# Optimization experiments

Hardware: AMD Instinct MI355X
Metric: run time of the kernel (lower is better)

Reference implementation:

```python
import jax, jax.numpy as jnp
import numpy as np

N_NODES = 100000
N_EDGES = 1600000
N_GRAPHS = 512
X_DIM = 4
H = 64
L = 3
NUM_CLASS = 3


def setup_inputs() -> dict:
    key = jax.random.key(0)
    ks = jax.random.split(key, 16)
    s = 0.1
    return {
        "x": jax.random.normal(ks[0], (N_NODES, X_DIM), jnp.float32),
        "edge_index": jax.random.randint(ks[1], (2, N_EDGES), 0, N_NODES, jnp.int64),
        "batch": jnp.sort(jax.random.randint(ks[2], (N_NODES,), 0, N_GRAPHS, jnp.int64)),
        "edge_attr": jax.random.uniform(ks[3], (N_EDGES,), jnp.float32),
        # node embedding
        "W_emb": jax.random.normal(ks[4], (X_DIM, H), jnp.float32) * s,
        "b_emb": jnp.zeros((H,), jnp.float32),
        # LEConv per-layer params (stacked over layers)
        "W1": jax.random.normal(ks[5], (L, H, H), jnp.float32) * s,
        "b1": jnp.zeros((L, H), jnp.float32),
        "W2": jax.random.normal(ks[6], (L, H, H), jnp.float32) * s,  # no bias (lin2)
        "W3": jax.random.normal(ks[7], (L, H, H), jnp.float32) * s,
        "b3": jnp.zeros((L, H), jnp.float32),
        # fc_out head
        "Wf1": jax.random.normal(ks[8], (H, 2 * H), jnp.float32) * s,
        "bf1": jnp.zeros((2 * H,), jnp.float32),
        "Wf2": jax.random.normal(ks[9], (2 * H, NUM_CLASS), jnp.float32) * s,
        "bf2": jnp.zeros((NUM_CLASS,), jnp.float32),
    }


def reference(x, edge_index, batch, edge_attr, W_emb, b_emb, W1, b1, W2, W3, b3,
              Wf1, bf1, Wf2, bf2):
    src, dst = edge_index[0], edge_index[1]
    # node embedding
    h = x @ W_emb + b_emb  # [N, H]
    # stacked LEConv layers: x_i' = sum_{j->i} e_ji * (lin1(x_j) - lin2(x_i)) + lin3(x_i)
    for l in range(L):
        a = h @ W1[l] + b1[l]          # [N, H]
        b = h @ W2[l]                  # [N, H] (lin2 has no bias)
        msg = (a[src] - b[dst]) * edge_attr[:, None]  # [E, H]
        agg = jax.ops.segment_sum(msg, dst, num_segments=N_NODES)
        h = jax.nn.relu(agg + h @ W3[l] + b3[l])
    # global mean pool per graph
    sums = jax.ops.segment_sum(h, batch, num_segments=N_GRAPHS)  # [G, H]
    cnt = jax.ops.segment_sum(jnp.ones((N_NODES,), h.dtype), batch, num_segments=N_GRAPHS)
    graph_x = sums / jnp.maximum(cnt, 1.0)[:, None]
    # fc_out head
    hid = jax.nn.relu(graph_x @ Wf1 + bf1)
    return hid @ Wf2 + bf2  # [G, NUM_CLASS]
```

## Files before the change

kernel.cpp:

```cpp
#include <hip/hip_runtime.h>

#define N_NODES 100000
#define N_EDGES 1600000
#define N_GRAPHS 512
#define X_DIM 4
#define H 64
#define LAYERS 3
#define NUM_CLASS 3
#define NBLK 256
#define EPB (N_EDGES / NBLK)
#define BKT_BITS 9
#define BKT_SZ 512
#define NBKT ((N_NODES + BKT_SZ - 1) / BKT_SZ)
#define MHIST (NBKT * NBLK)
#define NCH (MHIST / 512)
#define LROW 72
#define NCHUNKS ((N_NODES + 63) / 64)

typedef unsigned short ushort;
typedef short bf16x8 __attribute__((ext_vector_type(8)));
typedef unsigned short ush8 __attribute__((ext_vector_type(8)));
typedef float floatx4 __attribute__((ext_vector_type(4)));

__device__ __forceinline__ ushort f2bf(float v) {
    unsigned u = __float_as_uint(v);
    unsigned r = (u + 0x7fff + ((u >> 16) & 1)) >> 16;
    return (ushort)r;
}
__device__ __forceinline__ float bf2f(ushort s) {
    return __uint_as_float(((unsigned)s) << 16);
}

__global__ __launch_bounds__(256) void hist1_kernel(
    const int* __restrict__ dst, int* __restrict__ histM,
    const float* __restrict__ Wemb, const float* __restrict__ bemb,
    const float* __restrict__ W1, const float* __restrict__ b1,
    const float* __restrict__ W2, const float* __restrict__ W3,
    const float* __restrict__ b3,
    float* __restrict__ G, float* __restrict__ C) {
    __shared__ int hist[NBKT];
    int t = threadIdx.x, b = blockIdx.x;
    for (int i = t; i < NBKT; i += 256) hist[i] = 0;
    __syncthreads();
    int e0 = b * EPB;
    for (int j = t; j < EPB; j += 256) {
        int d = dst[e0 + j];
        atomicAdd(hist + (d >> BKT_BITS), 1);
    }
    __syncthreads();
    for (int i = t; i < NBKT; i += 256) histM[i * NBLK + b] = hist[i];
    if (b == 0 && t < H) {
        int f = t;
        const float* Ws[3] = {W1, W2, W3};
#pragma unroll
        for (int wsel = 0; wsel < 3; ++wsel) {
            const float* W = Ws[wsel];
#pragma unroll
            for (int c = 0; c < X_DIM; ++c) {
                float g = 0.f;
                for (int k = 0; k < H; ++k) g += Wemb[c * H + k] * W[k * H + f];
                G[wsel * 256 + c * H + f] = g;
            }
            float cb = (wsel == 0) ? b1[f] : (wsel == 2) ? b3[f] : 0.f;
            for (int k = 0; k < H; ++k) cb += bemb[k] * W[k * H + f];
            C[wsel * H + f] = cb;
        }
    }
}

__global__ __launch_bounds__(512) void gscan1_kernel(const int* __restrict__ v,
                                                     int* __restrict__ incl,
                                                     int* __restrict__ partials) {
    __shared__ int s[512];
    int tid = threadIdx.x;
    int i = blockIdx.x * 512 + tid;
    int x = (i < MHIST) ? v[i] : 0;
    s[tid] = x;
    for (int off = 1; off < 512; off <<= 1) {
        __syncthreads();
        int tv = (tid >= off) ? s[tid - off] : 0;
        __syncthreads();
        s[tid] += tv;
    }
    __syncthreads();
    if (i < MHIST) incl[i] = s[tid];
    if (tid == 511) partials[blockIdx.x] = s[tid];
}

__global__ __launch_bounds__(256) void scatter1_kernel(
    const int* __restrict__ src, const int* __restrict__ dst, const float* __restrict__ ea,
    const int* __restrict__ histM, const int* __restrict__ incl,
    const int* __restrict__ partials,
    unsigned* __restrict__ eb_se, int* __restrict__ eb_dst, int* __restrict__ bkt_ptr) {
    __shared__ int coff[128];
    __shared__ int cur[NBKT];
    int t = threadIdx.x, b = blockIdx.x;
    if (t < 128) coff[t] = (t < NCH) ? partials[t] : 0;
    __syncthreads();
    for (int off = 1; off < 128; off <<= 1) {
        int tv = (t < 128 && t >= off) ? coff[t - off] : 0;
        __syncthreads();
        if (t < 128) coff[t] += tv;
        __syncthreads();
    }
    for (int i = t; i < NBKT; i += 256) {
        int idx = i * NBLK + b;
        int ch = idx >> 9;
        int off0 = (ch == 0) ? 0 : coff[ch - 1];
        cur[i] = incl[idx] - histM[idx] + off0;
    }
    __syncthreads();
    if (b == 0) {
        for (int i = t; i < NBKT; i += 256) bkt_ptr[i] = cur[i];
        if (t == 0) bkt_ptr[NBKT] = N_EDGES;
    }
    int e0 = b * EPB;
    for (int j = t; j < EPB; j += 256) {
        int e = e0 + j;
        int d = dst[e];
        int k = d >> BKT_BITS;
        int pos = atomicAdd(cur + k, 1);
        eb_se[pos] = ((unsigned)src[e] << 15) | (unsigned)f2bf(ea[e]);
        eb_dst[pos] = d;
    }
}

__global__ __launch_bounds__(512) void bucket_kernel(
    const int* __restrict__ bkt_ptr, const unsigned* __restrict__ eb_se,
    const int* __restrict__ eb_dst,
    int* __restrict__ row_ptr, float* __restrict__ degw, unsigned* __restrict__ epack) {
    __shared__ int cnt[BKT_SZ];
    __shared__ float dws[BKT_SZ];
    __shared__ int s[BKT_SZ];
    __shared__ int cur[BKT_SZ];
    int k = blockIdx.x, t = threadIdx.x;
    int base = k << BKT_BITS;
    int nn = N_NODES - base;
    if (nn > BKT_SZ) nn = BKT_SZ;
    cnt[t] = 0;
    dws[t] = 0.0f;
    __syncthreads();
    int beg = bkt_ptr[k], end = bkt_ptr[k + 1];
    for (int j = beg + t; j < end; j += 512) {
        int d = eb_dst[j] - base;
        atomicAdd(cnt + d, 1);
        atomicAdd(dws + d, __uint_as_float((eb_se[j] & 0x7FFFu) << 16));
    }
    __syncthreads();
    s[t] = cnt[t];
    for (int off = 1; off < 512; off <<= 1) {
        __syncthreads();
        int tv = (t >= off) ? s[t - off] : 0;
        __syncthreads();
        s[t] += tv;
    }
    __syncthreads();
    int rstart = beg + s[t] - cnt[t];
    if (t < nn) {
        row_ptr[base + t] = rstart;
        degw[base + t] = dws[t];
        cur[t] = rstart;
    }
    __syncthreads();
    for (int j = beg + t; j < end; j += 512) {
        unsigned se = eb_se[j];
        int d = eb_dst[j] - base;
        int pos = atomicAdd(cur + d, 1);
        epack[pos] = se;
    }
    if (k == NBKT - 1 && t == 0) row_ptr[N_NODES] = N_EDGES;
}

__global__ __launch_bounds__(256) void layer1_kernel(
    const int* __restrict__ row_ptr, const unsigned* __restrict__ epack,
    const float* __restrict__ x, const float* __restrict__ degw,
    const float* __restrict__ G, const float* __restrict__ C,
    ushort* __restrict__ h) {
    int n = blockIdx.x * 4 + (threadIdx.x >> 6);
    if (n >= N_NODES) return;
    int lane = threadIdx.x & 63;
    float Gr[12], Cr[3];
#pragma unroll
    for (int i = 0; i < 12; ++i) Gr[i] = G[(i >> 2) * 256 + (i & 3) * 64 + lane];
#pragma unroll
    for (int i = 0; i < 3; ++i) Cr[i] = C[i * 64 + lane];
    int q2 = lane >> 1, cp = lane & 1;
    int beg = row_ptr[n], end = row_ptr[n + 1];
    float a0 = 0.f, a1 = 0.f;
    for (int j = beg; j < end; j += 32) {
        int jk = j + q2;
        unsigned w = (jk < end) ? epack[jk] : 0u;
        float2 xv = *(const float2*)&x[(size_t)(w >> 15) * X_DIM + cp * 2];
        float e = __uint_as_float((w & 0x7FFFu) << 16);
        a0 += e * xv.x;
        a1 += e * xv.y;
    }
#pragma unroll
    for (int mask = 2; mask <= 32; mask <<= 1) {
        a0 += __shfl_xor(a0, mask);
        a1 += __shfl_xor(a1, mask);
    }
    float mv0 = __shfl(a0, 0), mv1 = __shfl(a1, 0);
    float mv2 = __shfl(a0, 1), mv3 = __shfl(a1, 1);
    floatx4 xr = *(const floatx4*)&x[(size_t)n * X_DIM];
    float dw = degw[n];
    float t1 = mv0 * Gr[0] + mv1 * Gr[1] + mv2 * Gr[2] + mv3 * Gr[3];
    float t2 = xr[0] * Gr[4] + xr[1] * Gr[5] + xr[2] * Gr[6] + xr[3] * Gr[7];
    float t3 = xr[0] * Gr[8] + xr[1] * Gr[9] + xr[2] * Gr[10] + xr[3] * Gr[11];
    float v = t1 + dw * Cr[0] + t3 + Cr[2] - (t2 + Cr[1]) * dw;
    h[(size_t)n * H + lane] = f2bf(fmaxf(v, 0.0f));
}

__global__ __launch_bounds__(256) void gather_kernel(
    const int* __restrict__ row_ptr, const unsigned* __restrict__ epack,
    const ushort* __restrict__ h, ushort* __restrict__ m) {
    int n = blockIdx.x * 4 + (threadIdx.x >> 6);
    if (n >= N_NODES) return;
    int lane = threadIdx.x & 63;
    int q = lane >> 3, s = lane & 7;
    int beg = row_ptr[n], end = row_ptr[n + 1];
    float acc[8] = {0.f, 0.f, 0.f, 0.f, 0.f, 0.f, 0.f, 0.f};
    for (int j = beg; j < end; j += 32) {
        unsigned w[4];
#pragma unroll
        for (int k = 0; k < 4; ++k) {
            int jk = j + k * 8 + q;
            w[k] = (jk < end) ? epack[jk] : 0u;
        }
        ush8 av[4];
#pragma unroll
        for (int k = 0; k < 4; ++k)
            av[k] = *(const ush8*)&h[(size_t)(w[k] >> 15) * H + s * 8];
#pragma unroll
        for (int k = 0; k < 4; ++k) {
            float e = __uint_as_float((w[k] & 0x7FFFu) << 16);
#pragma unroll
            for (int i = 0; i < 8; ++i)
                acc[i] += e * bf2f((ushort)av[k][i]);
        }
    }
#pragma unroll
    for (int i = 0; i < 8; ++i) {
        acc[i] += __shfl_xor(acc[i], 8);
        acc[i] += __shfl_xor(acc[i], 16);
        acc[i] += __shfl_xor(acc[i], 32);
    }
    if (q == 0) {
        ush8 r;
#pragma unroll
        for (int i = 0; i < 8; ++i) r[i] = (short)f2bf(acc[i]);
        *(ush8*)&m[(size_t)n * H + s * 8] = r;
    }
}

__global__ __launch_bounds__(256) void linC_kernel(
    ushort* __restrict__ h, const ushort* __restrict__ m,
    const float* __restrict__ degw,
    const float* __restrict__ W1, const float* __restrict__ bias1,
    const float* __restrict__ W2, const float* __restrict__ W3,
    const float* __restrict__ bias3) {
    __shared__ alignas(16) ushort ah[64 * LROW];
    __shared__ alignas(16) ushort am[64 * LROW];
    int t = threadIdx.x;
    int wv = t >> 6, lane = t & 63;
    int quad = lane >> 4, m16 = lane & 15;
    int f = wv * 16 + m16;
    bf16x8 B[3][2][2];
    const float* Ws[3] = {W1, W2, W3};
#pragma unroll
    for (int wsel = 0; wsel < 3; ++wsel) {
#pragma unroll
        for (int kh = 0; kh < 2; ++kh) {
#pragma unroll
            for (int j = 0; j < 8; ++j) {
                float w = Ws[wsel][(kh * 32 + quad * 8 + j) * H + f];
                ushort hi = f2bf(w);
                B[wsel][kh][0][j] = (short)hi;
                B[wsel][kh][1][j] = (short)f2bf(w - bf2f(hi));
            }
        }
    }
    float bb1 = bias1[f], bb3 = bias3[f];
    for (int chunk = blockIdx.x; chunk < NCHUNKS; chunk += gridDim.x) {
        int nbase = chunk * 64;
        __syncthreads();
        for (int v = t; v < 64 * 8; v += 256) {
            int nl = v >> 3, k0 = (v & 7) * 8;
            int n = nbase + nl;
            ush8 vh = {0, 0, 0, 0, 0, 0, 0, 0};
            ush8 vm = {0, 0, 0, 0, 0, 0, 0, 0};
            if (n < N_NODES) {
                vh = *(const ush8*)&h[(size_t)n * H + k0];
                vm = *(const ush8*)&m[(size_t)n * H + k0];
            }
            *(ush8*)&ah[nl * LROW + k0] = vh;
            *(ush8*)&am[nl * LROW + k0] = vm;
        }
        __syncthreads();
#pragma unroll
        for (int ng = 0; ng < 4; ++ng) {
            int abase = (ng * 16 + m16) * LROW + quad * 8;
            bf16x8 Ah0 = *(const bf16x8*)&ah[abase];
            bf16x8 Ah1 = *(const bf16x8*)&ah[abase + 32];
            bf16x8 Am0 = *(const bf16x8*)&am[abase];
            bf16x8 Am1 = *(const bf16x8*)&am[abase + 32];
            floatx4 acc1 = {0.f, 0.f, 0.f, 0.f};
            floatx4 acc2 = {0.f, 0.f, 0.f, 0.f};
            floatx4 acc3 = {0.f, 0.f, 0.f, 0.f};
            acc1 = __builtin_amdgcn_mfma_f32_16x16x32_bf16(Am0, B[0][0][0], acc1, 0, 0, 0);
            acc1 = __builtin_amdgcn_mfma_f32_16x16x32_bf16(Am0, B[0][0][1], acc1, 0, 0, 0);
            acc1 = __builtin_amdgcn_mfma_f32_16x16x32_bf16(Am1, B[0][1][0], acc1, 0, 0, 0);
            acc1 = __builtin_amdgcn_mfma_f32_16x16x32_bf16(Am1, B[0][1][1], acc1, 0, 0, 0);
            acc2 = __builtin_amdgcn_mfma_f32_16x16x32_bf16(Ah0, B[1][0][0], acc2, 0, 0, 0);
            acc2 = __builtin_amdgcn_mfma_f32_16x16x32_bf16(Ah0, B[1][0][1], acc2, 0, 0, 0);
            acc2 = __builtin_amdgcn_mfma_f32_16x16x32_bf16(Ah1, B[1][1][0], acc2, 0, 0, 0);
            acc2 = __builtin_amdgcn_mfma_f32_16x16x32_bf16(Ah1, B[1][1][1], acc2, 0, 0, 0);
            acc3 = __builtin_amdgcn_mfma_f32_16x16x32_bf16(Ah0, B[2][0][0], acc3, 0, 0, 0);
            acc3 = __builtin_amdgcn_mfma_f32_16x16x32_bf16(Ah0, B[2][0][1], acc3, 0, 0, 0);
            acc3 = __builtin_amdgcn_mfma_f32_16x16x32_bf16(Ah1, B[2][1][0], acc3, 0, 0, 0);
            acc3 = __builtin_amdgcn_mfma_f32_16x16x32_bf16(Ah1, B[2][1][1], acc3, 0, 0, 0);
            int nrow = nbase + ng * 16 + quad * 4;
#pragma unroll
            for (int r = 0; r < 4; ++r) {
                int n = nrow + r;
                if (n < N_NODES) {
                    float dw = degw[n];
                    float v = acc1[r] + dw * bb1 + acc3[r] + bb3 - acc2[r] * dw;
                    h[(size_t)n * H + f] = f2bf(fmaxf(v, 0.0f));
                }
            }
        }
    }
}

__device__ __forceinline__ int lower_bound(const int* __restrict__ arr, int n, int key) {
    int lo = 0, hi = n;
    while (lo < hi) {
        int mid = (lo + hi) >> 1;
        if (arr[mid] < key) lo = mid + 1; else hi = mid;
    }
    return lo;
}

__global__ __launch_bounds__(256) void poolhead_kernel(
    const ushort* __restrict__ h, const int* __restrict__ batch,
    const float* __restrict__ Wf1, const float* __restrict__ bf1v,
    const float* __restrict__ Wf2, const float* __restrict__ bf2v,
    float* __restrict__ out) {
    __shared__ float psum[4][H];
    __shared__ float gx[H];
    __shared__ float hid[2 * H];
    int g = blockIdx.x, t = threadIdx.x;
    int s = lower_bound(batch, N_NODES, g);
    int e = lower_bound(batch, N_NODES, g + 1);
    int lane = t & 63, wv = t >> 6;
    int o = lane & 7;
    int nd = t >> 3;
    float acc[8] = {0.f, 0.f, 0.f, 0.f, 0.f, 0.f, 0.f, 0.f};
    for (int n = s + nd; n < e; n += 32) {
        ush8 v = *(const ush8*)&h[(size_t)n * H + o * 8];
#pragma unroll
        for (int i = 0; i < 8; ++i) acc[i] += bf2f((ushort)v[i]);
    }
#pragma unroll
    for (int i = 0; i < 8; ++i) {
        acc[i] += __shfl_xor(acc[i], 8);
        acc[i] += __shfl_xor(acc[i], 16);
        acc[i] += __shfl_xor(acc[i], 32);
    }
    if (lane < 8) {
#pragma unroll
        for (int i = 0; i < 8; ++i) psum[wv][o * 8 + i] = acc[i];
    }
    __syncthreads();
    if (t < H) {
        float c = (float)(e - s);
        gx[t] = (psum[0][t] + psum[1][t] + psum[2][t] + psum[3][t]) / fmaxf(c, 1.0f);
    }
    __syncthreads();
    if (t < 2 * H) {
        float acc2 = bf1v[t];
        for (int k = 0; k < H; ++k) acc2 += gx[k] * Wf1[k * 2 * H + t];
        hid[t] = fmaxf(acc2, 0.0f);
    }
    __syncthreads();
    if (t < NUM_CLASS) {
        float o2 = bf2v[t];
        for (int k = 0; k < 2 * H; ++k) o2 += hid[k] * Wf2[k * NUM_CLASS + t];
        out[g * NUM_CLASS + t] = o2;
    }
}

extern "C" void kernel_launch(void* const* d_in, const int* in_sizes, int n_in,
                              void* d_out, int out_size, void* d_ws, size_t ws_size,
                              hipStream_t stream) {
    const float* x    = (const float*)d_in[0];
    const int*  ei    = (const int*)d_in[1];
    const int*  batch = (const int*)d_in[2];
    const float* ea   = (const float*)d_in[3];
    const float* Wemb = (const float*)d_in[4];
    const float* bemb = (const float*)d_in[5];
    const float* pW1  = (const float*)d_in[6];
    const float* pb1  = (const float*)d_in[7];
    const float* pW2  = (const float*)d_in[8];
    const float* pW3  = (const float*)d_in[9];
    const float* pb3  = (const float*)d_in[10];
    const float* Wf1  = (const float*)d_in[11];
    const float* bf1v = (const float*)d_in[12];
    const float* Wf2  = (const float*)d_in[13];
    const float* bf2v = (const float*)d_in[14];
    float* out = (float*)d_out;

    const int* src = ei;
    const int* dst = ei + N_EDGES;

    const size_t NH = (size_t)N_NODES * H;
    char* p = (char*)d_ws;
    ushort* h       = (ushort*)p;            p += NH * 2;
    ushort* m       = (ushort*)p;            p += NH * 2;
    unsigned* epack = (unsigned*)p;          p += (size_t)N_EDGES * 4;
    int*   histM    = (int*)p;               p += MHIST * 4;
    int*   incl     = (int*)p;               p += MHIST * 4;
    int*   partials = (int*)p;               p += 512 * 4;
    int*   bkt_ptr  = (int*)p;               p += (NBKT + 1) * 4;
    int*   row_ptr  = (int*)p;               p += (N_NODES + 1) * 4;
    float* degw     = (float*)p;             p += N_NODES * 4;
    float* Gbuf     = (float*)p;             p += 3 * 256 * 4;
    float* Cbuf     = (float*)p;             p += 3 * 64 * 4;
    unsigned* eb_se = (unsigned*)m;
    int*     eb_dst = (int*)h;

    hist1_kernel<<<NBLK, 256, 0, stream>>>(dst, histM, Wemb, bemb, pW1, pb1, pW2, pW3, pb3,
                                           Gbuf, Cbuf);
    gscan1_kernel<<<MHIST / 512, 512, 0, stream>>>(histM, incl, partials);
    scatter1_kernel<<<NBLK, 256, 0, stream>>>(src, dst, ea, histM, incl, partials,
                                              eb_se, eb_dst, bkt_ptr);
    bucket_kernel<<<NBKT, 512, 0, stream>>>(bkt_ptr, eb_se, eb_dst, row_ptr, degw, epack);

    layer1_kernel<<<(N_NODES + 3) / 4, 256, 0, stream>>>(row_ptr, epack, x, degw,
                                                         Gbuf, Cbuf, h);

    for (int l = 1; l < LAYERS; ++l) {
        gather_kernel<<<(N_NODES + 3) / 4, 256, 0, stream>>>(row_ptr, epack, h, m);
        linC_kernel<<<512, 256, 0, stream>>>(
            h, m, degw,
            pW1 + (size_t)l * H * H, pb1 + (size_t)l * H,
            pW2 + (size_t)l * H * H,
            pW3 + (size_t)l * H * H, pb3 + (size_t)l * H);
    }

    poolhead_kernel<<<N_GRAPHS, 256, 0, stream>>>(h, batch, Wf1, bf1v, Wf2, bf2v, out);
}
```

Baseline: 315.4 us.

## Fuse neighbor gather and MFMA linear update into one per-layer kernel

Merges the gather kernel and the linear-combination kernel into a single kernel per layer. Each block gathers aggregated messages for its 64 nodes straight into shared memory, then runs the MFMA transforms. The h buffer is ping-ponged between two arrays so a layer never reads rows it is overwriting. This removes the round trip of the intermediate m array through global memory and one launch per layer. In exchange, each block now loads and splits its weights once per 64-node chunk instead of amortising them over a persistent grid, and each wave gathers 16 nodes serially, which may lower memory-level parallelism.

Result: slower. 342.5 us (+8.6%).

```diff
diff --git a/kernel.cpp b/kernel.cpp
--- a/kernel.cpp
+++ b/kernel.cpp
@@ -211,50 +211,9 @@
     h[(size_t)n * H + lane] = f2bf(fmaxf(v, 0.0f));
 }
 
-__global__ __launch_bounds__(256) void gather_kernel(
+__global__ __launch_bounds__(256) void fused_layer_kernel(
+    const ushort* __restrict__ hin, ushort* __restrict__ hout,
     const int* __restrict__ row_ptr, const unsigned* __restrict__ epack,
-    const ushort* __restrict__ h, ushort* __restrict__ m) {
-    int n = blockIdx.x * 4 + (threadIdx.x >> 6);
-    if (n >= N_NODES) return;
-    int lane = threadIdx.x & 63;
-    int q = lane >> 3, s = lane & 7;
-    int beg = row_ptr[n], end = row_ptr[n + 1];
-    float acc[8] = {0.f, 0.f, 0.f, 0.f, 0.f, 0.f, 0.f, 0.f};
-    for (int j = beg; j < end; j += 32) {
-        unsigned w[4];
-#pragma unroll
-        for (int k = 0; k < 4; ++k) {
-            int jk = j + k * 8 + q;
-            w[k] = (jk < end) ? epack[jk] : 0u;
-        }
-        ush8 av[4];
-#pragma unroll
-        for (int k = 0; k < 4; ++k)
-            av[k] = *(const ush8*)&h[(size_t)(w[k] >> 15) * H + s * 8];
-#pragma unroll
-        for (int k = 0; k < 4; ++k) {
-            float e = __uint_as_float((w[k] & 0x7FFFu) << 16);
-#pragma unroll
-            for (int i = 0; i < 8; ++i)
-                acc[i] += e * bf2f((ushort)av[k][i]);
-        }
-    }
-#pragma unroll
-    for (int i = 0; i < 8; ++i) {
-        acc[i] += __shfl_xor(acc[i], 8);
-        acc[i] += __shfl_xor(acc[i], 16);
-        acc[i] += __shfl_xor(acc[i], 32);
-    }
-    if (q == 0) {
-        ush8 r;
-#pragma unroll
-        for (int i = 0; i < 8; ++i) r[i] = (short)f2bf(acc[i]);
-        *(ush8*)&m[(size_t)n * H + s * 8] = r;
-    }
-}
-
-__global__ __launch_bounds__(256) void linC_kernel(
-    ushort* __restrict__ h, const ushort* __restrict__ m,
     const float* __restrict__ degw,
     const float* __restrict__ W1, const float* __restrict__ bias1,
     const float* __restrict__ W2, const float* __restrict__ W3,
@@ -264,7 +223,7 @@
     int t = threadIdx.x;
     int wv = t >> 6, lane = t & 63;
     int quad = lane >> 4, m16 = lane & 15;
-    int f = wv * 16 + m16;
+    int fcol = wv * 16 + m16;
     bf16x8 B[3][2][2];
     const float* Ws[3] = {W1, W2, W3};
 #pragma unroll
@@ -273,61 +232,95 @@
         for (int kh = 0; kh < 2; ++kh) {
 #pragma unroll
             for (int j = 0; j < 8; ++j) {
-                float w = Ws[wsel][(kh * 32 + quad * 8 + j) * H + f];
+                float w = Ws[wsel][(kh * 32 + quad * 8 + j) * H + fcol];
                 ushort hi = f2bf(w);
                 B[wsel][kh][0][j] = (short)hi;
                 B[wsel][kh][1][j] = (short)f2bf(w - bf2f(hi));
             }
         }
     }
-    float bb1 = bias1[f], bb3 = bias3[f];
-    for (int chunk = blockIdx.x; chunk < NCHUNKS; chunk += gridDim.x) {
-        int nbase = chunk * 64;
-        __syncthreads();
-        for (int v = t; v < 64 * 8; v += 256) {
-            int nl = v >> 3, k0 = (v & 7) * 8;
+    float bb1 = bias1[fcol], bb3 = bias3[fcol];
+    int nbase = blockIdx.x * 64;
+    for (int v = t; v < 64 * 8; v += 256) {
+        int nl = v >> 3, k0 = (v & 7) * 8;
+        int n = nbase + nl;
+        ush8 val = {0, 0, 0, 0, 0, 0, 0, 0};
+        if (n < N_NODES) val = *(const ush8*)&hin[(size_t)n * H + k0];
+        *(ush8*)&ah[nl * LROW + k0] = val;
+    }
+    {
+        int q = lane >> 3, s = lane & 7;
+        for (int i = 0; i < 16; ++i) {
+            int nl = wv * 16 + i;
             int n = nbase + nl;
-            ush8 vh = {0, 0, 0, 0, 0, 0, 0, 0};
-            ush8 vm = {0, 0, 0, 0, 0, 0, 0, 0};
+            float acc[8] = {0.f, 0.f, 0.f, 0.f, 0.f, 0.f, 0.f, 0.f};
             if (n < N_NODES) {
-                vh = *(const ush8*)&h[(size_t)n * H + k0];
-                vm = *(const ush8*)&m[(size_t)n * H + k0];
-            }
-            *(ush8*)&ah[nl * LROW + k0] = vh;
-            *(ush8*)&am[nl * LROW + k0] = vm;
+                int beg = row_ptr[n], end = row_ptr[n + 1];
+                for (int j = beg; j < end; j += 32) {
+                    unsigned w[4];
+#pragma unroll
+                    for (int k = 0; k < 4; ++k) {
+                        int jk = j + k * 8 + q;
+                        w[k] = (jk < end) ? epack[jk] : 0u;
+                    }
+                    ush8 av[4];
+#pragma unroll
+                    for (int k = 0; k < 4; ++k)
+                        av[k] = *(const ush8*)&hin[(size_t)(w[k] >> 15) * H + s * 8];
+#pragma unroll
+                    for (int k = 0; k < 4; ++k) {
+                        float e = __uint_as_float((w[k] & 0x7FFFu) << 16);
+#pragma unroll
+                        for (int ii = 0; ii < 8; ++ii)
+                            acc[ii] += e * bf2f((ushort)av[k][ii]);
+                    }
+                }
+            }
+#pragma unroll
+            for (int ii = 0; ii < 8; ++ii) {
+                acc[ii] += __shfl_xor(acc[ii], 8);
+                acc[ii] += __shfl_xor(acc[ii], 16);
+                acc[ii] += __shfl_xor(acc[ii], 32);
+            }
+            if (q == 0) {
+                ush8 r;
+#pragma unroll
+                for (int ii = 0; ii < 8; ++ii) r[ii] = (short)f2bf(acc[ii]);
+                *(ush8*)&am[nl * LROW + s * 8] = r;
+            }
         }
-        __syncthreads();
-#pragma unroll
-        for (int ng = 0; ng < 4; ++ng) {
-            int abase = (ng * 16 + m16) * LROW + quad * 8;
-            bf16x8 Ah0 = *(const bf16x8*)&ah[abase];
-            bf16x8 Ah1 = *(const bf16x8*)&ah[abase + 32];
-            bf16x8 Am0 = *(const bf16x8*)&am[abase];
-            bf16x8 Am1 = *(const bf16x8*)&am[abase + 32];
-            floatx4 acc1 = {0.f, 0.f, 0.f, 0.f};
-            floatx4 acc2 = {0.f, 0.f, 0.f, 0.f};
-            floatx4 acc3 = {0.f, 0.f, 0.f, 0.f};
-            acc1 = __builtin_amdgcn_mfma_f32_16x16x32_bf16(Am0, B[0][0][0], acc1, 0, 0, 0);
-            acc1 = __builtin_amdgcn_mfma_f32_16x16x32_bf16(Am0, B[0][0][1], acc1, 0, 0, 0);
-            acc1 = __builtin_amdgcn_mfma_f32_16x16x32_bf16(Am1, B[0][1][0], acc1, 0, 0, 0);
-            acc1 = __builtin_amdgcn_mfma_f32_16x16x32_bf16(Am1, B[0][1][1], acc1, 0, 0, 0);
-            acc2 = __builtin_amdgcn_mfma_f32_16x16x32_bf16(Ah0, B[1][0][0], acc2, 0, 0, 0);
-            acc2 = __builtin_amdgcn_mfma_f32_16x16x32_bf16(Ah0, B[1][0][1], acc2, 0, 0, 0);
-            acc2 = __builtin_amdgcn_mfma_f32_16x16x32_bf16(Ah1, B[1][1][0], acc2, 0, 0, 0);
-            acc2 = __builtin_amdgcn_mfma_f32_16x16x32_bf16(Ah1, B[1][1][1], acc2, 0, 0, 0);
-            acc3 = __builtin_amdgcn_mfma_f32_16x16x32_bf16(Ah0, B[2][0][0], acc3, 0, 0, 0);
-            acc3 = __builtin_amdgcn_mfma_f32_16x16x32_bf16(Ah0, B[2][0][1], acc3, 0, 0, 0);
-            acc3 = __builtin_amdgcn_mfma_f32_16x16x32_bf16(Ah1, B[2][1][0], acc3, 0, 0, 0);
-            acc3 = __builtin_amdgcn_mfma_f32_16x16x32_bf16(Ah1, B[2][1][1], acc3, 0, 0, 0);
-            int nrow = nbase + ng * 16 + quad * 4;
-#pragma unroll
-            for (int r = 0; r < 4; ++r) {
-                int n = nrow + r;
-                if (n < N_NODES) {
-                    float dw = degw[n];
-                    float v = acc1[r] + dw * bb1 + acc3[r] + bb3 - acc2[r] * dw;
-                    h[(size_t)n * H + f] = f2bf(fmaxf(v, 0.0f));
-                }
+    }
+    __syncthreads();
+#pragma unroll
+    for (int ng = 0; ng < 4; ++ng) {
+        int abase = (ng * 16 + m16) * LROW + quad * 8;
+        bf16x8 Ah0 = *(const bf16x8*)&ah[abase];
+        bf16x8 Ah1 = *(const bf16x8*)&ah[abase + 32];
+        bf16x8 Am0 = *(const bf16x8*)&am[abase];
+        bf16x8 Am1 = *(const bf16x8*)&am[abase + 32];
+        floatx4 acc1 = {0.f, 0.f, 0.f, 0.f};
+        floatx4 acc2 = {0.f, 0.f, 0.f, 0.f};
+        floatx4 acc3 = {0.f, 0.f, 0.f, 0.f};
+        acc1 = __builtin_amdgcn_mfma_f32_16x16x32_bf16(Am0, B[0][0][0], acc1, 0, 0, 0);
+        acc1 = __builtin_amdgcn_mfma_f32_16x16x32_bf16(Am0, B[0][0][1], acc1, 0, 0, 0);
+        acc1 = __builtin_amdgcn_mfma_f32_16x16x32_bf16(Am1, B[0][1][0], acc1, 0, 0, 0);
+        acc1 = __builtin_amdgcn_mfma_f32_16x16x32_bf16(Am1, B[0][1][1], acc1, 0, 0, 0);
+        acc2 = __builtin_amdgcn_mfma_f32_16x16x32_bf16(Ah0, B[1][0][0], acc2, 0, 0, 0);
+        acc2 = __builtin_amdgcn_mfma_f32_16x16x32_bf16(Ah0, B[1][0][1], acc2, 0, 0, 0);
+        acc2 = __builtin_amdgcn_mfma_f32_16x16x32_bf16(Ah1, B[1][1][0], acc2, 0, 0, 0);
+        acc2 = __builtin_amdgcn_mfma_f32_16x16x32_bf16(Ah1, B[1][1][1], acc2, 0, 0, 0);
+        acc3 = __builtin_amdgcn_mfma_f32_16x16x32_bf16(Ah0, B[2][0][0], acc3, 0, 0, 0);
+        acc3 = __builtin_amdgcn_mfma_f32_16x16x32_bf16(Ah0, B[2][0][1], acc3, 0, 0, 0);
+        acc3 = __builtin_amdgcn_mfma_f32_16x16x32_bf16(Ah1, B[2][1][0], acc3, 0, 0, 0);
+        acc3 = __builtin_amdgcn_mfma_f32_16x16x32_bf16(Ah1, B[2][1][1], acc3, 0, 0, 0);
+        int nrow = nbase + ng * 16 + quad * 4;
+#pragma unroll
+        for (int r = 0; r < 4; ++r) {
+            int n = nrow + r;
+            if (n < N_NODES) {
+                float dw = degw[n];
+                float v = acc1[r] + dw * bb1 + acc3[r] + bb3 - acc2[r] * dw;
+                hout[(size_t)n * H + fcol] = f2bf(fmaxf(v, 0.0f));
             }
         }
     }
@@ -416,8 +409,8 @@
 
     const size_t NH = (size_t)N_NODES * H;
     char* p = (char*)d_ws;
-    ushort* h       = (ushort*)p;            p += NH * 2;
-    ushort* m       = (ushort*)p;            p += NH * 2;
+    ushort* hA      = (ushort*)p;            p += NH * 2;
+    ushort* hB      = (ushort*)p;            p += NH * 2;
     unsigned* epack = (unsigned*)p;          p += (size_t)N_EDGES * 4;
     int*   histM    = (int*)p;               p += MHIST * 4;
     int*   incl     = (int*)p;               p += MHIST * 4;
@@ -427,8 +420,8 @@
     float* degw     = (float*)p;             p += N_NODES * 4;
     float* Gbuf     = (float*)p;             p += 3 * 256 * 4;
     float* Cbuf     = (float*)p;             p += 3 * 64 * 4;
-    unsigned* eb_se = (unsigned*)m;
-    int*     eb_dst = (int*)h;
+    unsigned* eb_se = (unsigned*)hB;
+    int*     eb_dst = (int*)hA;
 
     hist1_kernel<<<NBLK, 256, 0, stream>>>(dst, histM, Wemb, bemb, pW1, pb1, pW2, pW3, pb3,
                                            Gbuf, Cbuf);
@@ -438,16 +431,16 @@
     bucket_kernel<<<NBKT, 512, 0, stream>>>(bkt_ptr, eb_se, eb_dst, row_ptr, degw, epack);
 
     layer1_kernel<<<(N_NODES + 3) / 4, 256, 0, stream>>>(row_ptr, epack, x, degw,
-                                                         Gbuf, Cbuf, h);
-
-    for (int l = 1; l < LAYERS; ++l) {
-        gather_kernel<<<(N_NODES + 3) / 4, 256, 0, stream>>>(row_ptr, epack, h, m);
-        linC_kernel<<<512, 256, 0, stream>>>(
-            h, m, degw,
-            pW1 + (size_t)l * H * H, pb1 + (size_t)l * H,
-            pW2 + (size_t)l * H * H,
-            pW3 + (size_t)l * H * H, pb3 + (size_t)l * H);
-    }
-
-    poolhead_kernel<<<N_GRAPHS, 256, 0, stream>>>(h, batch, Wf1, bf1v, Wf2, bf2v, out);
-}
+                                                         Gbuf, Cbuf, hA);
+
+    fused_layer_kernel<<<NCHUNKS, 256, 0, stream>>>(
+        hA, hB, row_ptr, epack, degw,
+        pW1 + (size_t)1 * H * H, pb1 + (size_t)1 * H,
+        pW2 + (size_t)1 * H * H, pW3 + (size_t)1 * H * H, pb3 + (size_t)1 * H);
+    fused_layer_kernel<<<NCHUNKS, 256, 0, stream>>>(
+        hB, hA, row_ptr, epack, degw,
+        pW1 + (size_t)2 * H * H, pb1 + (size_t)2 * H,
+        pW2 + (size_t)2 * H * H, pW3 + (size_t)2 * H * H, pb3 + (size_t)2 * H);
+
+    poolhead_kernel<<<N_GRAPHS, 256, 0, stream>>>(hA, batch, Wf1, bf1v, Wf2, bf2v, out);
+}
```

## Fuse first-layer aggregation into bucket CSR-build kernel

Applied to the files above, without the earlier changes.

The separate layer1 kernel, which re-read the CSR edges and gathered x per node, is removed. Its work moves into bucket_kernel, which now accumulates edge-weighted x sums per destination node with shared-memory atomics while it builds the CSR, then computes and writes the first-layer h for its bucket. This saves one kernel launch and a second pass over the edge list, at the cost of four extra float atomics per edge in LDS and more shared memory per block. The eb_dst staging buffer moves into m so it no longer aliases h, which is now written inside the same kernel.

After: 353.0 us. +11.9%, slower.

```diff
diff --git a/kernel.cpp b/kernel.cpp
--- a/kernel.cpp
+++ b/kernel.cpp
@@ -127,24 +127,37 @@
 
 __global__ __launch_bounds__(512) void bucket_kernel(
     const int* __restrict__ bkt_ptr, const unsigned* __restrict__ eb_se,
-    const int* __restrict__ eb_dst,
-    int* __restrict__ row_ptr, float* __restrict__ degw, unsigned* __restrict__ epack) {
+    const int* __restrict__ eb_dst, const float* __restrict__ x,
+    const float* __restrict__ G, const float* __restrict__ C,
+    int* __restrict__ row_ptr, float* __restrict__ degw, unsigned* __restrict__ epack,
+    ushort* __restrict__ h) {
     __shared__ int cnt[BKT_SZ];
     __shared__ float dws[BKT_SZ];
     __shared__ int s[BKT_SZ];
     __shared__ int cur[BKT_SZ];
+    __shared__ float mxs[BKT_SZ * X_DIM];
+    __shared__ float Gs[768], Cs[192];
     int k = blockIdx.x, t = threadIdx.x;
     int base = k << BKT_BITS;
     int nn = N_NODES - base;
     if (nn > BKT_SZ) nn = BKT_SZ;
     cnt[t] = 0;
     dws[t] = 0.0f;
+#pragma unroll
+    for (int i = 0; i < X_DIM; ++i) mxs[i * BKT_SZ + t] = 0.0f;
+    for (int i = t; i < 768; i += 512) Gs[i] = G[i];
+    if (t < 192) Cs[t] = C[t];
     __syncthreads();
     int beg = bkt_ptr[k], end = bkt_ptr[k + 1];
     for (int j = beg + t; j < end; j += 512) {
+        unsigned se = eb_se[j];
         int d = eb_dst[j] - base;
+        float e = __uint_as_float((se & 0x7FFFu) << 16);
         atomicAdd(cnt + d, 1);
-        atomicAdd(dws + d, __uint_as_float((eb_se[j] & 0x7FFFu) << 16));
+        atomicAdd(dws + d, e);
+        floatx4 xv = *(const floatx4*)&x[(size_t)(se >> 15) * X_DIM];
+#pragma unroll
+        for (int c = 0; c < X_DIM; ++c) atomicAdd(mxs + c * BKT_SZ + d, e * xv[c]);
     }
     __syncthreads();
     s[t] = cnt[t];
@@ -169,46 +182,21 @@
         epack[pos] = se;
     }
     if (k == NBKT - 1 && t == 0) row_ptr[N_NODES] = N_EDGES;
-}
-
-__global__ __launch_bounds__(256) void layer1_kernel(
-    const int* __restrict__ row_ptr, const unsigned* __restrict__ epack,
-    const float* __restrict__ x, const float* __restrict__ degw,
-    const float* __restrict__ G, const float* __restrict__ C,
-    ushort* __restrict__ h) {
-    int n = blockIdx.x * 4 + (threadIdx.x >> 6);
-    if (n >= N_NODES) return;
-    int lane = threadIdx.x & 63;
-    float Gr[12], Cr[3];
-#pragma unroll
-    for (int i = 0; i < 12; ++i) Gr[i] = G[(i >> 2) * 256 + (i & 3) * 64 + lane];
-#pragma unroll
-    for (int i = 0; i < 3; ++i) Cr[i] = C[i * 64 + lane];
-    int q2 = lane >> 1, cp = lane & 1;
-    int beg = row_ptr[n], end = row_ptr[n + 1];
-    float a0 = 0.f, a1 = 0.f;
-    for (int j = beg; j < end; j += 32) {
-        int jk = j + q2;
-        unsigned w = (jk < end) ? epack[jk] : 0u;
-        float2 xv = *(const float2*)&x[(size_t)(w >> 15) * X_DIM + cp * 2];
-        float e = __uint_as_float((w & 0x7FFFu) << 16);
-        a0 += e * xv.x;
-        a1 += e * xv.y;
-    }
-#pragma unroll
-    for (int mask = 2; mask <= 32; mask <<= 1) {
-        a0 += __shfl_xor(a0, mask);
-        a1 += __shfl_xor(a1, mask);
-    }
-    float mv0 = __shfl(a0, 0), mv1 = __shfl(a1, 0);
-    float mv2 = __shfl(a0, 1), mv3 = __shfl(a1, 1);
-    floatx4 xr = *(const floatx4*)&x[(size_t)n * X_DIM];
-    float dw = degw[n];
-    float t1 = mv0 * Gr[0] + mv1 * Gr[1] + mv2 * Gr[2] + mv3 * Gr[3];
-    float t2 = xr[0] * Gr[4] + xr[1] * Gr[5] + xr[2] * Gr[6] + xr[3] * Gr[7];
-    float t3 = xr[0] * Gr[8] + xr[1] * Gr[9] + xr[2] * Gr[10] + xr[3] * Gr[11];
-    float v = t1 + dw * Cr[0] + t3 + Cr[2] - (t2 + Cr[1]) * dw;
-    h[(size_t)n * H + lane] = f2bf(fmaxf(v, 0.0f));
+    for (int i = t; i < nn * H; i += 512) {
+        int nl = i >> 6, f = i & 63;
+        float dw = dws[nl];
+        floatx4 xv = *(const floatx4*)&x[(size_t)(base + nl) * X_DIM];
+        float t1 = 0.f, t2 = 0.f, t3 = 0.f;
+#pragma unroll
+        for (int c = 0; c < X_DIM; ++c) {
+            float mv = mxs[c * BKT_SZ + nl];
+            t1 += mv * Gs[c * 64 + f];
+            t2 += xv[c] * Gs[256 + c * 64 + f];
+            t3 += xv[c] * Gs[512 + c * 64 + f];
+        }
+        float v = t1 + dw * Cs[f] + t3 + Cs[128 + f] - (t2 + Cs[64 + f]) * dw;
+        h[(size_t)(base + nl) * H + f] = f2bf(fmaxf(v, 0.0f));
+    }
 }
 
 __global__ __launch_bounds__(256) void gather_kernel(
@@ -428,17 +416,15 @@
     float* Gbuf     = (float*)p;             p += 3 * 256 * 4;
     float* Cbuf     = (float*)p;             p += 3 * 64 * 4;
     unsigned* eb_se = (unsigned*)m;
-    int*     eb_dst = (int*)h;
+    int*     eb_dst = (int*)((char*)m + (size_t)N_EDGES * 4);
 
     hist1_kernel<<<NBLK, 256, 0, stream>>>(dst, histM, Wemb, bemb, pW1, pb1, pW2, pW3, pb3,
                                            Gbuf, Cbuf);
     gscan1_kernel<<<MHIST / 512, 512, 0, stream>>>(histM, incl, partials);
     scatter1_kernel<<<NBLK, 256, 0, stream>>>(src, dst, ea, histM, incl, partials,
                                               eb_se, eb_dst, bkt_ptr);
-    bucket_kernel<<<NBKT, 512, 0, stream>>>(bkt_ptr, eb_se, eb_dst, row_ptr, degw, epack);
-
-    layer1_kernel<<<(N_NODES + 3) / 4, 256, 0, stream>>>(row_ptr, epack, x, degw,
-                                                         Gbuf, Cbuf, h);
+    bucket_kernel<<<NBKT, 512, 0, stream>>>(bkt_ptr, eb_se, eb_dst, x, Gbuf, Cbuf,
+                                            row_ptr, degw, epack, h);
 
     for (int l = 1; l < LAYERS; ++l) {
         gather_kernel<<<(N_NODES + 3) / 4, 256, 0, stream>>>(row_ptr, epack, h, m);
```
